# Kernel tuning notes

Measured on AMD Instinct MI355X. Metric: run time of the kernel, lower is better.

## Reference

```python
import jax, jax.numpy as jnp
import numpy as np
import math

SCALED = True
SUBSEQUENT_MASK = True
B, SQ, SK, D, DV = 8, 2048, 2048, 1024, 1024


def _build_mask(query_lens, key_lens, sq, sk, causal):
    # (B, Sq, Sk) boolean validity mask: rows >= q_len and cols >= k_len are masked.
    qm = jnp.arange(sq)[None, :, None] < query_lens[:, None, None]
    km = jnp.arange(sk)[None, None, :] < key_lens[:, None, None]
    mask = qm & km
    if causal:
        mask = mask & (jnp.arange(sk)[None, None, :] <= jnp.arange(sq)[None, :, None])
    return mask


def _masked_softmax(scores, mask):
    # Stable masked softmax; fully-masked rows yield exactly 0 (matches the
    # original's NaN -> 0 replacement) without producing NaNs.
    neg = jnp.finfo(scores.dtype).min
    s = jnp.where(mask, scores, neg)
    m = jnp.max(s, axis=-1, keepdims=True)
    e = jnp.where(mask, jnp.exp(s - m), jnp.zeros((), scores.dtype))
    denom = jnp.sum(e, axis=-1, keepdims=True)
    return e / jnp.where(denom == 0, jnp.ones((), scores.dtype), denom)


def setup_inputs() -> dict:
    key = jax.random.key(0)
    kq, kk, kv, kql, kkl = jax.random.split(key, 5)
    return {
        "queries": jax.random.normal(kq, (B, SQ, D), dtype=jnp.float32),
        "keys": jax.random.normal(kk, (B, SK, D), dtype=jnp.float32),
        "values": jax.random.normal(kv, (B, SK, DV), dtype=jnp.float32),
        "query_lens": jax.random.randint(kql, (B,), 1, SQ + 1),
        "key_lens": jax.random.randint(kkl, (B,), 1, SK + 1),
    }


def reference(queries, keys, values, query_lens, key_lens):
    # scores: (B, Sq, Sk)
    scores = jnp.einsum("bqd,bkd->bqk", queries, keys)
    if SCALED:
        scores = scores / math.sqrt(queries.shape[2])
    mask = _build_mask(query_lens, key_lens, queries.shape[1], keys.shape[1], SUBSEQUENT_MASK)
    weights = _masked_softmax(scores, mask)
    context = jnp.einsum("bqk,bkv->bqv", weights, values)
    return (context, weights)
```

## Files before the change

### kernel.cpp

```cpp
#include <hip/hip_runtime.h>
#include <hip/hip_bf16.h>

#define B_   8
#define SQ_  2048
#define SK_  2048
#define D_   1024
#define DV_  1024

typedef __bf16 bf16;
typedef __attribute__((ext_vector_type(4))) __bf16 bf16x4;
typedef __attribute__((ext_vector_type(8))) __bf16 bf16x8;
typedef __attribute__((ext_vector_type(4))) float  f32x4;

__global__ __launch_bounds__(512, 4)
void scores_kernel(const float* __restrict__ Q, const float* __restrict__ K,
                   const int* __restrict__ qlens, const int* __restrict__ klens,
                   float* __restrict__ Wout)
{
    const int b  = blockIdx.z;
    const int q0 = blockIdx.y * 128;
    const int k0 = blockIdx.x * 128;
    if (k0 > q0 + 127) return;
    const int qlen = qlens[b], klen = klens[b];
    if (q0 >= qlen || k0 >= klen) return;

    __shared__ __align__(16) bf16 Qs[2][128][72];
    __shared__ __align__(16) bf16 Ks[2][128][72];

    const int tid  = threadIdx.x;
    const int lane = tid & 63;
    const int w    = tid >> 6;
    const int wq   = w >> 1, wk = w & 1;

    const float* Qb = Q + (size_t)b * SQ_ * D_;
    const float* Kb = K + (size_t)b * SK_ * D_;

    float4 qreg[4], kreg[4];
    int srow[4], sc4[4];
    #pragma unroll
    for (int i = 0; i < 4; ++i) {
        int s = tid + i * 512;
        srow[i] = s >> 4;
        sc4[i]  = (s & 15) << 2;
    }

    auto load_tile = [&](int d0) {
        #pragma unroll
        for (int i = 0; i < 4; ++i) {
            qreg[i] = *(const float4*)(Qb + (size_t)(q0 + srow[i]) * D_ + d0 + sc4[i]);
            kreg[i] = *(const float4*)(Kb + (size_t)(k0 + srow[i]) * D_ + d0 + sc4[i]);
        }
    };
    auto store_tile = [&](int buf) {
        #pragma unroll
        for (int i = 0; i < 4; ++i) {
            bf16x4 qb = { (bf16)qreg[i].x, (bf16)qreg[i].y, (bf16)qreg[i].z, (bf16)qreg[i].w };
            bf16x4 kb = { (bf16)kreg[i].x, (bf16)kreg[i].y, (bf16)kreg[i].z, (bf16)kreg[i].w };
            *(bf16x4*)&Qs[buf][srow[i]][sc4[i]] = qb;
            *(bf16x4*)&Ks[buf][srow[i]][sc4[i]] = kb;
        }
    };

    f32x4 acc[2][4] = {};

    load_tile(0);
    store_tile(0);
    __syncthreads();

    for (int it = 0; it < 16; ++it) {
        const int cur = it & 1;
        if (it < 15) load_tile((it + 1) * 64);
        #pragma unroll
        for (int kk = 0; kk < 2; ++kk) {
            const int koff = kk * 32 + ((lane >> 4) << 3);
            bf16x8 a[2], bb[4];
            #pragma unroll
            for (int m = 0; m < 2; ++m)
                a[m] = *(const bf16x8*)&Qs[cur][32 * wq + 16 * m + (lane & 15)][koff];
            #pragma unroll
            for (int n = 0; n < 4; ++n)
                bb[n] = *(const bf16x8*)&Ks[cur][64 * wk + 16 * n + (lane & 15)][koff];
            #pragma unroll
            for (int m = 0; m < 2; ++m)
                #pragma unroll
                for (int n = 0; n < 4; ++n)
                    acc[m][n] = __builtin_amdgcn_mfma_f32_16x16x32_bf16(a[m], bb[n], acc[m][n], 0, 0, 0);
        }
        if (it < 15) store_tile(1 - cur);
        __syncthreads();
    }

    float* Wb = Wout + (size_t)b * SQ_ * SK_;
    const int rb = q0 + 32 * wq + ((lane >> 4) << 2);
    const int cb = k0 + 64 * wk + (lane & 15);
    #pragma unroll
    for (int m = 0; m < 2; ++m)
        #pragma unroll
        for (int n = 0; n < 4; ++n)
            #pragma unroll
            for (int r = 0; r < 4; ++r)
                Wb[(size_t)(rb + 16 * m + r) * SK_ + (cb + 16 * n)] = acc[m][n][r] * 0.03125f;
}

__global__ __launch_bounds__(256)
void softmax_kernel(const int* __restrict__ qlens, const int* __restrict__ klens,
                    float* __restrict__ W)
{
    const int bq = blockIdx.x;
    const int b  = bq >> 11;
    const int q  = bq & 2047;
    const int qlen = qlens[b], klen = klens[b];
    int kmax = 0;
    if (q < qlen) kmax = min(klen, q + 1);

    float4* row = (float4*)(W + (size_t)bq * SK_);
    const int tid = threadIdx.x;

    float4 x[2];
    float m = -INFINITY;
    #pragma unroll
    for (int i = 0; i < 2; ++i) {
        int v4 = tid + i * 256;
        int kb = v4 << 2;
        if (kb < kmax) x[i] = row[v4];
        else           x[i] = make_float4(-INFINITY, -INFINITY, -INFINITY, -INFINITY);
        float* xe = (float*)&x[i];
        #pragma unroll
        for (int e = 0; e < 4; ++e) {
            if (kb + e >= kmax) xe[e] = -INFINITY;
            m = fmaxf(m, xe[e]);
        }
    }
    #pragma unroll
    for (int off = 32; off > 0; off >>= 1) m = fmaxf(m, __shfl_xor(m, off, 64));
    __shared__ float red[4];
    if ((tid & 63) == 0) red[tid >> 6] = m;
    __syncthreads();
    m = fmaxf(fmaxf(red[0], red[1]), fmaxf(red[2], red[3]));
    __syncthreads();

    float sum = 0.f;
    #pragma unroll
    for (int i = 0; i < 2; ++i) {
        float* xe = (float*)&x[i];
        #pragma unroll
        for (int e = 0; e < 4; ++e) {
            float ev = (xe[e] == -INFINITY) ? 0.f : __expf(xe[e] - m);
            xe[e] = ev;
            sum += ev;
        }
    }
    #pragma unroll
    for (int off = 32; off > 0; off >>= 1) sum += __shfl_xor(sum, off, 64);
    if ((tid & 63) == 0) red[tid >> 6] = sum;
    __syncthreads();
    sum = red[0] + red[1] + red[2] + red[3];

    const float inv = (sum > 0.f) ? (1.f / sum) : 0.f;
    #pragma unroll
    for (int i = 0; i < 2; ++i) {
        float* xe = (float*)&x[i];
        float4 o = { xe[0] * inv, xe[1] * inv, xe[2] * inv, xe[3] * inv };
        row[tid + i * 256] = o;
    }
}

__global__ __launch_bounds__(512, 4)
void context_kernel(const float* __restrict__ W, const float* __restrict__ V,
                    const int* __restrict__ klens, float* __restrict__ Out)
{
    const int b  = blockIdx.z;
    const int q0 = blockIdx.y * 128;
    const int n0 = blockIdx.x * 128;
    const int klen = klens[b];
    const int kend = min(q0 + 128, (klen + 63) & ~63);
    const int nk   = kend >> 6;

    __shared__ __align__(16) bf16 Ws[2][128][72];
    __shared__ __align__(16) bf16 Vs[2][128][72];

    const int tid  = threadIdx.x;
    const int lane = tid & 63;
    const int w    = tid >> 6;
    const int wq   = w >> 1, wn = w & 1;

    const float* Wb = W + (size_t)b * SQ_ * SK_;
    const float* Vb = V + (size_t)b * SK_ * DV_;

    float4 wreg[4];
    float  vreg[2][8];
    int srow[4], sc4[4], vn[2], voct[2];
    #pragma unroll
    for (int i = 0; i < 4; ++i) {
        int s = tid + i * 512;
        srow[i] = s >> 4;
        sc4[i]  = (s & 15) << 2;
    }
    #pragma unroll
    for (int i = 0; i < 2; ++i) {
        int t = tid + i * 512;
        vn[i]   = t & 127;
        voct[i] = t >> 7;
    }

    auto load_tile = [&](int kk0) {
        #pragma unroll
        for (int i = 0; i < 4; ++i)
            wreg[i] = *(const float4*)(Wb + (size_t)(q0 + srow[i]) * SK_ + kk0 + sc4[i]);
        #pragma unroll
        for (int i = 0; i < 2; ++i)
            #pragma unroll
            for (int j = 0; j < 8; ++j)
                vreg[i][j] = Vb[(size_t)(kk0 + voct[i] * 8 + j) * DV_ + n0 + vn[i]];
    };
    auto store_tile = [&](int buf) {
        #pragma unroll
        for (int i = 0; i < 4; ++i) {
            bf16x4 wb = { (bf16)wreg[i].x, (bf16)wreg[i].y, (bf16)wreg[i].z, (bf16)wreg[i].w };
            *(bf16x4*)&Ws[buf][srow[i]][sc4[i]] = wb;
        }
        #pragma unroll
        for (int i = 0; i < 2; ++i) {
            bf16x8 vb = { (bf16)vreg[i][0], (bf16)vreg[i][1], (bf16)vreg[i][2], (bf16)vreg[i][3],
                          (bf16)vreg[i][4], (bf16)vreg[i][5], (bf16)vreg[i][6], (bf16)vreg[i][7] };
            *(bf16x8*)&Vs[buf][vn[i]][voct[i] * 8] = vb;
        }
    };

    f32x4 acc[2][4] = {};

    load_tile(0);
    store_tile(0);
    __syncthreads();

    for (int it = 0; it < nk; ++it) {
        const int cur = it & 1;
        if (it + 1 < nk) load_tile((it + 1) * 64);
        #pragma unroll
        for (int kk = 0; kk < 2; ++kk) {
            const int koff = kk * 32 + ((lane >> 4) << 3);
            bf16x8 a[2], bb[4];
            #pragma unroll
            for (int m = 0; m < 2; ++m)
                a[m] = *(const bf16x8*)&Ws[cur][32 * wq + 16 * m + (lane & 15)][koff];
            #pragma unroll
            for (int n = 0; n < 4; ++n)
                bb[n] = *(const bf16x8*)&Vs[cur][64 * wn + 16 * n + (lane & 15)][koff];
            #pragma unroll
            for (int m = 0; m < 2; ++m)
                #pragma unroll
                for (int n = 0; n < 4; ++n)
                    acc[m][n] = __builtin_amdgcn_mfma_f32_16x16x32_bf16(a[m], bb[n], acc[m][n], 0, 0, 0);
        }
        if (it + 1 < nk) store_tile(1 - cur);
        __syncthreads();
    }

    float* Ob = Out + (size_t)b * SQ_ * DV_;
    const int rb = q0 + 32 * wq + ((lane >> 4) << 2);
    const int cb = n0 + 64 * wn + (lane & 15);
    #pragma unroll
    for (int m = 0; m < 2; ++m)
        #pragma unroll
        for (int n = 0; n < 4; ++n)
            #pragma unroll
            for (int r = 0; r < 4; ++r)
                Ob[(size_t)(rb + 16 * m + r) * DV_ + (cb + 16 * n)] = acc[m][n][r];
}

extern "C" void kernel_launch(void* const* d_in, const int* in_sizes, int n_in,
                              void* d_out, int out_size, void* d_ws, size_t ws_size,
                              hipStream_t stream) {
    (void)in_sizes; (void)n_in; (void)out_size; (void)d_ws; (void)ws_size;
    const float* Q     = (const float*)d_in[0];
    const float* K     = (const float*)d_in[1];
    const float* V     = (const float*)d_in[2];
    const int*   qlens = (const int*)d_in[3];
    const int*   klens = (const int*)d_in[4];

    float* ctx = (float*)d_out;
    float* wts = ctx + (size_t)B_ * SQ_ * DV_;

    dim3 g1(SK_ / 128, SQ_ / 128, B_);
    scores_kernel<<<g1, 512, 0, stream>>>(Q, K, qlens, klens, wts);

    softmax_kernel<<<dim3(B_ * SQ_), 256, 0, stream>>>(qlens, klens, wts);

    dim3 g3(DV_ / 128, SQ_ / 128, B_);
    context_kernel<<<g3, 512, 0, stream>>>(wts, V, klens, ctx);
}
```

Before: 472.3 us.

## Pre-transpose V to bf16, emit bf16 weights, async-copy context tiles to LDS

A new kernel transposes V into a bf16 workspace buffer, laid out row-major along the key dimension. The softmax kernel now also writes a bf16 copy of the weights. The context GEMM then reads both operands as contiguous bf16 and streams them into unpadded LDS with global_load_lds direct copies. This replaces the per-element strided fp32 V gathers and the register conversions that staged data into shared memory. The scores kernel also moves to 64x64 tiles with 256 threads, for finer causal skipping and more blocks. The costs are an extra transpose pass, extra bf16 weight writes, possible LDS bank conflicts from the unpadded layout, and lower reuse in the smaller scores tiles.

```diff
diff --git a/kernel.cpp b/kernel.cpp
--- a/kernel.cpp
+++ b/kernel.cpp
@@ -1,5 +1,6 @@
 #include <hip/hip_runtime.h>
 #include <hip/hip_bf16.h>
+#include <stdint.h>
 
 #define B_   8
 #define SQ_  2048
@@ -12,25 +13,61 @@
 typedef __attribute__((ext_vector_type(8))) __bf16 bf16x8;
 typedef __attribute__((ext_vector_type(4))) float  f32x4;
 
-__global__ __launch_bounds__(512, 4)
+__device__ __forceinline__ void async_cp16(const void* g, void* l) {
+    __builtin_amdgcn_global_load_lds((const __attribute__((address_space(1))) void*)g,
+                                     (__attribute__((address_space(3))) void*)l,
+                                     16, 0, 0);
+}
+
+__global__ __launch_bounds__(256)
+void vtrans_kernel(const float* __restrict__ V, bf16* __restrict__ Vt)
+{
+    const int b  = blockIdx.z;
+    const int n0 = blockIdx.y * 64;
+    const int k0 = blockIdx.x * 64;
+    __shared__ float L[64][65];
+    const int tid = threadIdx.x;
+    const float* Vb = V + (size_t)b * SK_ * DV_;
+    #pragma unroll
+    for (int i = 0; i < 4; ++i) {
+        int s = tid + i * 256;
+        int kr = s >> 4, n4 = (s & 15) << 2;
+        float4 v = *(const float4*)(Vb + (size_t)(k0 + kr) * DV_ + n0 + n4);
+        L[kr][n4 + 0] = v.x; L[kr][n4 + 1] = v.y;
+        L[kr][n4 + 2] = v.z; L[kr][n4 + 3] = v.w;
+    }
+    __syncthreads();
+    bf16* Vtb = Vt + (size_t)b * DV_ * SK_;
+    #pragma unroll
+    for (int i = 0; i < 2; ++i) {
+        int u = tid + i * 256;
+        int nr = u >> 3, kc = (u & 7) << 3;
+        bf16x8 o = { (bf16)L[kc + 0][nr], (bf16)L[kc + 1][nr],
+                     (bf16)L[kc + 2][nr], (bf16)L[kc + 3][nr],
+                     (bf16)L[kc + 4][nr], (bf16)L[kc + 5][nr],
+                     (bf16)L[kc + 6][nr], (bf16)L[kc + 7][nr] };
+        *(bf16x8*)(Vtb + (size_t)(n0 + nr) * SK_ + k0 + kc) = o;
+    }
+}
+
+__global__ __launch_bounds__(256)
 void scores_kernel(const float* __restrict__ Q, const float* __restrict__ K,
                    const int* __restrict__ qlens, const int* __restrict__ klens,
                    float* __restrict__ Wout)
 {
     const int b  = blockIdx.z;
-    const int q0 = blockIdx.y * 128;
-    const int k0 = blockIdx.x * 128;
-    if (k0 > q0 + 127) return;
+    const int q0 = blockIdx.y * 64;
+    const int k0 = blockIdx.x * 64;
+    if (k0 > q0 + 63) return;
     const int qlen = qlens[b], klen = klens[b];
     if (q0 >= qlen || k0 >= klen) return;
 
-    __shared__ __align__(16) bf16 Qs[2][128][72];
-    __shared__ __align__(16) bf16 Ks[2][128][72];
+    __shared__ __align__(16) bf16 Qs[2][64][72];
+    __shared__ __align__(16) bf16 Ks[2][64][72];
 
     const int tid  = threadIdx.x;
     const int lane = tid & 63;
     const int w    = tid >> 6;
-    const int wq   = w >> 1, wk = w & 1;
 
     const float* Qb = Q + (size_t)b * SQ_ * D_;
     const float* Kb = K + (size_t)b * SK_ * D_;
@@ -39,7 +76,7 @@
     int srow[4], sc4[4];
     #pragma unroll
     for (int i = 0; i < 4; ++i) {
-        int s = tid + i * 512;
+        int s = tid + i * 256;
         srow[i] = s >> 4;
         sc4[i]  = (s & 15) << 2;
     }
@@ -61,7 +98,7 @@
         }
     };
 
-    f32x4 acc[2][4] = {};
+    f32x4 acc[4] = {};
 
     load_tile(0);
     store_tile(0);
@@ -73,38 +110,30 @@
         #pragma unroll
         for (int kk = 0; kk < 2; ++kk) {
             const int koff = kk * 32 + ((lane >> 4) << 3);
-            bf16x8 a[2], bb[4];
-            #pragma unroll
-            for (int m = 0; m < 2; ++m)
-                a[m] = *(const bf16x8*)&Qs[cur][32 * wq + 16 * m + (lane & 15)][koff];
-            #pragma unroll
-            for (int n = 0; n < 4; ++n)
-                bb[n] = *(const bf16x8*)&Ks[cur][64 * wk + 16 * n + (lane & 15)][koff];
-            #pragma unroll
-            for (int m = 0; m < 2; ++m)
-                #pragma unroll
-                for (int n = 0; n < 4; ++n)
-                    acc[m][n] = __builtin_amdgcn_mfma_f32_16x16x32_bf16(a[m], bb[n], acc[m][n], 0, 0, 0);
+            bf16x8 a = *(const bf16x8*)&Qs[cur][16 * w + (lane & 15)][koff];
+            #pragma unroll
+            for (int n = 0; n < 4; ++n) {
+                bf16x8 bb = *(const bf16x8*)&Ks[cur][16 * n + (lane & 15)][koff];
+                acc[n] = __builtin_amdgcn_mfma_f32_16x16x32_bf16(a, bb, acc[n], 0, 0, 0);
+            }
         }
         if (it < 15) store_tile(1 - cur);
         __syncthreads();
     }
 
     float* Wb = Wout + (size_t)b * SQ_ * SK_;
-    const int rb = q0 + 32 * wq + ((lane >> 4) << 2);
-    const int cb = k0 + 64 * wk + (lane & 15);
-    #pragma unroll
-    for (int m = 0; m < 2; ++m)
-        #pragma unroll
-        for (int n = 0; n < 4; ++n)
-            #pragma unroll
-            for (int r = 0; r < 4; ++r)
-                Wb[(size_t)(rb + 16 * m + r) * SK_ + (cb + 16 * n)] = acc[m][n][r] * 0.03125f;
+    const int rb = q0 + 16 * w + ((lane >> 4) << 2);
+    const int cb = k0 + (lane & 15);
+    #pragma unroll
+    for (int n = 0; n < 4; ++n)
+        #pragma unroll
+        for (int r = 0; r < 4; ++r)
+            Wb[(size_t)(rb + r) * SK_ + (cb + 16 * n)] = acc[n][r] * 0.03125f;
 }
 
 __global__ __launch_bounds__(256)
 void softmax_kernel(const int* __restrict__ qlens, const int* __restrict__ klens,
-                    float* __restrict__ W)
+                    float* __restrict__ W, bf16* __restrict__ Wb16)
 {
     const int bq = blockIdx.x;
     const int b  = bq >> 11;
@@ -114,6 +143,7 @@
     if (q < qlen) kmax = min(klen, q + 1);
 
     float4* row = (float4*)(W + (size_t)bq * SK_);
+    bf16*  rowb = Wb16 + (size_t)bq * SK_;
     const int tid = threadIdx.x;
 
     float4 x[2];
@@ -162,11 +192,13 @@
         float* xe = (float*)&x[i];
         float4 o = { xe[0] * inv, xe[1] * inv, xe[2] * inv, xe[3] * inv };
         row[tid + i * 256] = o;
-    }
-}
-
-__global__ __launch_bounds__(512, 4)
-void context_kernel(const float* __restrict__ W, const float* __restrict__ V,
+        bf16x4 ob = { (bf16)o.x, (bf16)o.y, (bf16)o.z, (bf16)o.w };
+        *(bf16x4*)(rowb + (size_t)(tid + i * 256) * 4) = ob;
+    }
+}
+
+__global__ __launch_bounds__(512)
+void context_kernel(const bf16* __restrict__ Wb16, const bf16* __restrict__ Vt,
                     const int* __restrict__ klens, float* __restrict__ Out)
 {
     const int b  = blockIdx.z;
@@ -176,84 +208,53 @@
     const int kend = min(q0 + 128, (klen + 63) & ~63);
     const int nk   = kend >> 6;
 
-    __shared__ __align__(16) bf16 Ws[2][128][72];
-    __shared__ __align__(16) bf16 Vs[2][128][72];
+    __shared__ __align__(16) bf16 As[2][128][64];
+    __shared__ __align__(16) bf16 Bs[2][128][64];
 
     const int tid  = threadIdx.x;
     const int lane = tid & 63;
     const int w    = tid >> 6;
     const int wq   = w >> 1, wn = w & 1;
 
-    const float* Wb = W + (size_t)b * SQ_ * SK_;
-    const float* Vb = V + (size_t)b * SK_ * DV_;
-
-    float4 wreg[4];
-    float  vreg[2][8];
-    int srow[4], sc4[4], vn[2], voct[2];
-    #pragma unroll
-    for (int i = 0; i < 4; ++i) {
-        int s = tid + i * 512;
-        srow[i] = s >> 4;
-        sc4[i]  = (s & 15) << 2;
-    }
-    #pragma unroll
-    for (int i = 0; i < 2; ++i) {
-        int t = tid + i * 512;
-        vn[i]   = t & 127;
-        voct[i] = t >> 7;
-    }
-
-    auto load_tile = [&](int kk0) {
-        #pragma unroll
-        for (int i = 0; i < 4; ++i)
-            wreg[i] = *(const float4*)(Wb + (size_t)(q0 + srow[i]) * SK_ + kk0 + sc4[i]);
-        #pragma unroll
-        for (int i = 0; i < 2; ++i)
-            #pragma unroll
-            for (int j = 0; j < 8; ++j)
-                vreg[i][j] = Vb[(size_t)(kk0 + voct[i] * 8 + j) * DV_ + n0 + vn[i]];
+    const bf16* Ab = Wb16 + (size_t)b * SQ_ * SK_;
+    const bf16* Bb = Vt   + (size_t)b * DV_ * SK_;
+
+    const int lrow = w * 8 + (lane >> 3);
+    const int lcol = (lane & 7) << 3;
+
+    auto issue = [&](int buf, int k0) {
+        #pragma unroll
+        for (int i = 0; i < 2; ++i) {
+            async_cp16(Ab + (size_t)(q0 + i * 64 + lrow) * SK_ + k0 + lcol,
+                       &As[buf][i * 64 + w * 8][0]);
+            async_cp16(Bb + (size_t)(n0 + i * 64 + lrow) * SK_ + k0 + lcol,
+                       &Bs[buf][i * 64 + w * 8][0]);
+        }
     };
-    auto store_tile = [&](int buf) {
-        #pragma unroll
-        for (int i = 0; i < 4; ++i) {
-            bf16x4 wb = { (bf16)wreg[i].x, (bf16)wreg[i].y, (bf16)wreg[i].z, (bf16)wreg[i].w };
-            *(bf16x4*)&Ws[buf][srow[i]][sc4[i]] = wb;
-        }
-        #pragma unroll
-        for (int i = 0; i < 2; ++i) {
-            bf16x8 vb = { (bf16)vreg[i][0], (bf16)vreg[i][1], (bf16)vreg[i][2], (bf16)vreg[i][3],
-                          (bf16)vreg[i][4], (bf16)vreg[i][5], (bf16)vreg[i][6], (bf16)vreg[i][7] };
-            *(bf16x8*)&Vs[buf][vn[i]][voct[i] * 8] = vb;
-        }
-    };
 
     f32x4 acc[2][4] = {};
 
-    load_tile(0);
-    store_tile(0);
-    __syncthreads();
-
+    issue(0, 0);
     for (int it = 0; it < nk; ++it) {
         const int cur = it & 1;
-        if (it + 1 < nk) load_tile((it + 1) * 64);
+        __syncthreads();
+        if (it + 1 < nk) issue(1 - cur, (it + 1) * 64);
         #pragma unroll
         for (int kk = 0; kk < 2; ++kk) {
             const int koff = kk * 32 + ((lane >> 4) << 3);
             bf16x8 a[2], bb[4];
             #pragma unroll
             for (int m = 0; m < 2; ++m)
-                a[m] = *(const bf16x8*)&Ws[cur][32 * wq + 16 * m + (lane & 15)][koff];
+                a[m] = *(const bf16x8*)&As[cur][32 * wq + 16 * m + (lane & 15)][koff];
             #pragma unroll
             for (int n = 0; n < 4; ++n)
-                bb[n] = *(const bf16x8*)&Vs[cur][64 * wn + 16 * n + (lane & 15)][koff];
+                bb[n] = *(const bf16x8*)&Bs[cur][64 * wn + 16 * n + (lane & 15)][koff];
             #pragma unroll
             for (int m = 0; m < 2; ++m)
                 #pragma unroll
                 for (int n = 0; n < 4; ++n)
                     acc[m][n] = __builtin_amdgcn_mfma_f32_16x16x32_bf16(a[m], bb[n], acc[m][n], 0, 0, 0);
         }
-        if (it + 1 < nk) store_tile(1 - cur);
-        __syncthreads();
     }
 
     float* Ob = Out + (size_t)b * SQ_ * DV_;
@@ -271,7 +272,7 @@
 extern "C" void kernel_launch(void* const* d_in, const int* in_sizes, int n_in,
                               void* d_out, int out_size, void* d_ws, size_t ws_size,
                               hipStream_t stream) {
-    (void)in_sizes; (void)n_in; (void)out_size; (void)d_ws; (void)ws_size;
+    (void)in_sizes; (void)n_in; (void)out_size; (void)ws_size;
     const float* Q     = (const float*)d_in[0];
     const float* K     = (const float*)d_in[1];
     const float* V     = (const float*)d_in[2];
@@ -281,11 +282,14 @@
     float* ctx = (float*)d_out;
     float* wts = ctx + (size_t)B_ * SQ_ * DV_;
 
-    dim3 g1(SK_ / 128, SQ_ / 128, B_);
-    scores_kernel<<<g1, 512, 0, stream>>>(Q, K, qlens, klens, wts);
-
-    softmax_kernel<<<dim3(B_ * SQ_), 256, 0, stream>>>(qlens, klens, wts);
-
-    dim3 g3(DV_ / 128, SQ_ / 128, B_);
-    context_kernel<<<g3, 512, 0, stream>>>(wts, V, klens, ctx);
-}
+    bf16* Vt   = (bf16*)d_ws;
+    bf16* Wb16 = Vt + (size_t)B_ * DV_ * SK_;
+
+    vtrans_kernel<<<dim3(SK_ / 64, DV_ / 64, B_), 256, 0, stream>>>(V, Vt);
+
+    scores_kernel<<<dim3(SK_ / 64, SQ_ / 64, B_), 256, 0, stream>>>(Q, K, qlens, klens, wts);
+
+    softmax_kernel<<<dim3(B_ * SQ_), 256, 0, stream>>>(qlens, klens, wts, Wb16);
+
+    context_kernel<<<dim3(DV_ / 128, SQ_ / 128, B_), 512, 0, stream>>>(Wb16, Vt, klens, ctx);
+}
```

Result: slower. 503.8 us (+6.7%).
